# Kernel tuning notes

Hardware: AMD Instinct MI355X
Metric: run time of the kernel (lower is better)

Reference implementation:

```python
import jax, jax.numpy as jnp
import numpy as np

USR_NUM = 100000
D_IN = 32
D_HID = 32
D_MID = 16
D_OUT = 2
N_EDGES = 1600000
EPS = 1e-16  # matches torch_geometric.utils.softmax denominator eps


def _glorot(key, shape):
    fan_in, fan_out = shape[0], shape[1]
    lim = np.sqrt(6.0 / (fan_in + fan_out))
    return jax.random.uniform(key, shape, jnp.float32, -lim, lim)


def setup_inputs() -> dict:
    key = jax.random.key(0)
    ks = jax.random.split(key, 16)
    inp = {
        "edge_index": jax.random.randint(ks[0], (2, N_EDGES), 0, USR_NUM, dtype=jnp.int64)
        if jax.config.jax_enable_x64 else jax.random.randint(ks[0], (2, N_EDGES), 0, USR_NUM).astype(jnp.int32),
        "emb": jax.random.normal(ks[1], (USR_NUM, D_IN), jnp.float32),
        # conv1: TransformerConv(32 -> 32, heads=1)
        "Wq1": _glorot(ks[2], (D_IN, D_HID)), "bq1": jnp.zeros((D_HID,), jnp.float32),
        "Wk1": _glorot(ks[3], (D_IN, D_HID)), "bk1": jnp.zeros((D_HID,), jnp.float32),
        "Wv1": _glorot(ks[4], (D_IN, D_HID)), "bv1": jnp.zeros((D_HID,), jnp.float32),
        "Ws1": _glorot(ks[5], (D_IN, D_HID)), "bs1": jnp.zeros((D_HID,), jnp.float32),
        # conv2: TransformerConv(32 -> 16, heads=1)
        "Wq2": _glorot(ks[6], (D_HID, D_MID)), "bq2": jnp.zeros((D_MID,), jnp.float32),
        "Wk2": _glorot(ks[7], (D_HID, D_MID)), "bk2": jnp.zeros((D_MID,), jnp.float32),
        "Wv2": _glorot(ks[8], (D_HID, D_MID)), "bv2": jnp.zeros((D_MID,), jnp.float32),
        "Ws2": _glorot(ks[9], (D_HID, D_MID)), "bs2": jnp.zeros((D_MID,), jnp.float32),
        # output: Linear(16 -> 2)
        "Wo": _glorot(ks[10], (D_MID, D_OUT)), "bo": jnp.zeros((D_OUT,), jnp.float32),
    }
    return inp


def transformer_conv(x, src, dst, Wq, bq, Wk, bk, Wv, bv, Ws, bs, n_nodes):
    # edge (j=src -> i=dst): alpha_ij = softmax_i( <q_i, k_j> / sqrt(d) )
    d = Wq.shape[1]
    q = (x @ Wq + bq)[dst]          # [E, d]
    k = (x @ Wk + bk)[src]          # [E, d]
    v = (x @ Wv + bv)[src]          # [E, d]
    alpha = jnp.sum(q * k, axis=-1) / jnp.sqrt(jnp.float32(d))  # [E]
    # segment softmax over incoming edges of each destination node
    seg_max = jax.ops.segment_max(alpha, dst, num_segments=n_nodes)  # [N]
    e = jnp.exp(alpha - seg_max[dst])
    seg_sum = jax.ops.segment_sum(e, dst, num_segments=n_nodes)      # [N]
    w = e / (seg_sum[dst] + EPS)
    agg = jax.ops.segment_sum(v * w[:, None], dst, num_segments=n_nodes)  # [N, d]
    return agg + x @ Ws + bs  # root/skip connection (PyG default root_weight=True)


def reference(edge_index, emb,
              Wq1, bq1, Wk1, bk1, Wv1, bv1, Ws1, bs1,
              Wq2, bq2, Wk2, bk2, Wv2, bv2, Ws2, bs2,
              Wo, bo):
    src, dst = edge_index[0], edge_index[1]
    h = transformer_conv(emb, src, dst, Wq1, bq1, Wk1, bk1, Wv1, bv1, Ws1, bs1, USR_NUM)
    h = jax.nn.relu(h)
    h = transformer_conv(h, src, dst, Wq2, bq2, Wk2, bk2, Wv2, bv2, Ws2, bs2, USR_NUM)
    h = jax.nn.relu(h)
    return h @ Wo + bo  # [N, 2]
```

## Files before the change

### kernel.cpp

```cpp
#include <hip/hip_runtime.h>
#include <hip/hip_bf16.h>

typedef __hip_bfloat16 bf16;
typedef unsigned int uint;
typedef unsigned short ushort;

#define N_NODES 100000
#define N_EDGES_C 1600000
#define NSB 196
#define NSBP 200
#define SBCAP 10240
#define RND 2048
#define EPB (RND / 256)
#define NBIN 64
#define G_RAD ((N_EDGES_C + RND - 1) / RND)
#define NHB 392
#define HCAP 5632
#define NSLOT (NHB * 256)

__device__ __forceinline__ float ldf(const void* p, long i, int isbf) {
    return isbf ? __bfloat162float(((const bf16*)p)[i]) : ((const float*)p)[i];
}
__device__ __forceinline__ int ldidx(const int* ei, long pos, int is64) {
    return is64 ? ei[2 * pos] : ei[pos];
}
__device__ __forceinline__ ushort bfb(float x) {
    bf16 h = __float2bfloat16(x);
    return *(ushort*)&h;
}
__device__ __forceinline__ float bl(uint u) { return __uint_as_float(u << 16); }
__device__ __forceinline__ float bh(uint u) { return __uint_as_float(u & 0xFFFF0000u); }

__global__ void setup_kernel(
    const void* emb, const int* ei,
    const void* Wq1, const void* bq1, const void* Wk1, const void* bk1,
    const void* Wv1, const void* bv1, const void* Ws1, const void* bs1,
    const void* Wq2, const void* bq2, const void* Wk2, const void* bk2,
    const void* Wv2, const void* bv2, const void* Ws2, const void* bs2,
    const void* Wo, const void* bo,
    int* flags, float* wp1, float* bp1, float* wp2, float* bp2, float* woF,
    int* curSB) {
    __shared__ int sf0;
    int t = threadIdx.x;
    if (t < 64) {
        const bf16* pb = (const bf16*)emb;
        int bad = 0;
        for (int i = t; i < 256; i += 64) {
            float v = __bfloat162float(pb[i]);
            if (!(v > -1.0e6f && v < 1.0e6f)) bad++;
        }
        int nz = 0;
        for (int i = 2 * t + 1; i < 256; i += 128) nz += (ei[i] != 0) ? 1 : 0;
#pragma unroll
        for (int m = 32; m >= 1; m >>= 1) {
            bad += __shfl_xor(bad, m, 64);
            nz  += __shfl_xor(nz, m, 64);
        }
        if (t == 0) {
            int f0 = (bad <= 8) ? 1 : 0;
            flags[0] = f0;
            flags[1] = (nz == 0) ? 1 : 0;
            sf0 = f0;
        }
    }
    __syncthreads();
    int isbf = sf0;
    for (int i = t; i < 1024; i += 256) {
        wp1[i]        = ldf(Wq1, i, isbf);
        wp1[1024 + i] = ldf(Wk1, i, isbf);
        wp1[2048 + i] = ldf(Wv1, i, isbf);
        wp1[3072 + i] = ldf(Ws1, i, isbf);
    }
    for (int i = t; i < 512; i += 256) {
        wp2[i]        = ldf(Wq2, i, isbf);
        wp2[512 + i]  = ldf(Wk2, i, isbf);
        wp2[1024 + i] = ldf(Wv2, i, isbf);
        wp2[1536 + i] = ldf(Ws2, i, isbf);
    }
    if (t < 32) {
        bp1[t] = ldf(bq1, t, isbf); bp1[32 + t] = ldf(bk1, t, isbf);
        bp1[64 + t] = ldf(bv1, t, isbf); bp1[96 + t] = ldf(bs1, t, isbf);
        woF[t] = ldf(Wo, t, isbf);
    }
    if (t < 16) {
        bp2[t] = ldf(bq2, t, isbf); bp2[16 + t] = ldf(bk2, t, isbf);
        bp2[32 + t] = ldf(bv2, t, isbf); bp2[48 + t] = ldf(bs2, t, isbf);
    }
    if (t < 2) woF[32 + t] = ldf(bo, t, isbf);
    curSB[t] = 0;
}

template <int DOUT, bool RUNTIME_DTYPE>
__device__ __forceinline__ void node_linear_body(
    const void* __restrict__ X, const float* __restrict__ wpack,
    const float* __restrict__ bpack, const int* __restrict__ flags,
    float* __restrict__ q, ushort* __restrict__ kvb, float* __restrict__ s,
    int bid, float* __restrict__ sW, float* __restrict__ sbias, float* __restrict__ sX) {
    const int TPN = DOUT / 4;
    const int NPB = 256 / TPN;
    const int W_ELEMS = 4 * 32 * DOUT;

    const float4* wp4 = (const float4*)wpack;
    float4* sW4 = (float4*)sW;
    for (int i = threadIdx.x; i < W_ELEMS / 4; i += 256) sW4[i] = wp4[i];
    if (threadIdx.x < 4 * DOUT) sbias[threadIdx.x] = bpack[threadIdx.x];
    const int base = bid * NPB * 32;
    bool useBf = RUNTIME_DTYPE && (flags[0] != 0);
    if (useBf) {
        for (int i = threadIdx.x; i < NPB * 32; i += 256) {
            int g = base + i;
            float xv = (g < N_NODES * 32) ? __bfloat162float(((const bf16*)X)[g]) : 0.0f;
            sX[(i >> 5) * 36 + (i & 31)] = xv;
        }
    } else {
        for (int i = threadIdx.x; i < NPB * 32; i += 256) {
            int g = base + i;
            sX[(i >> 5) * 36 + (i & 31)] = (g < N_NODES * 32) ? ((const float*)X)[g] : 0.0f;
        }
    }
    __syncthreads();

    int l = threadIdx.x / TPN;
    int c4 = (threadIdx.x % TPN) * 4;
    int n = bid * NPB + l;
    if (n >= N_NODES) return;

    float xr[32];
#pragma unroll
    for (int j = 0; j < 8; j++) {
        float4 t4 = *(const float4*)&sX[l * 36 + 4 * j];
        xr[4 * j] = t4.x; xr[4 * j + 1] = t4.y; xr[4 * j + 2] = t4.z; xr[4 * j + 3] = t4.w;
    }
    float acc[4][4];
#pragma unroll
    for (int m = 0; m < 4; m++)
#pragma unroll
        for (int j = 0; j < 4; j++) acc[m][j] = sbias[m * DOUT + c4 + j];

#pragma unroll
    for (int t = 0; t < 32; t++) {
#pragma unroll
        for (int m = 0; m < 4; m++) {
            float4 w = *(const float4*)&sW[(m * 32 + t) * DOUT + c4];
            acc[m][0] += xr[t] * w.x;
            acc[m][1] += xr[t] * w.y;
            acc[m][2] += xr[t] * w.z;
            acc[m][3] += xr[t] * w.w;
        }
    }
    size_t o = (size_t)n * DOUT + c4;
    *(float4*)&q[o] = make_float4(acc[0][0], acc[0][1], acc[0][2], acc[0][3]);
    *(float4*)&s[o] = make_float4(acc[3][0], acc[3][1], acc[3][2], acc[3][3]);
    size_t okv = (size_t)n * 2 * DOUT + c4;
    ushort4 kp = make_ushort4(bfb(acc[1][0]), bfb(acc[1][1]), bfb(acc[1][2]), bfb(acc[1][3]));
    ushort4 vp = make_ushort4(bfb(acc[2][0]), bfb(acc[2][1]), bfb(acc[2][2]), bfb(acc[2][3]));
    *(ushort4*)&kvb[okv]        = kp;
    *(ushort4*)&kvb[okv + DOUT] = vp;
}

struct RadixS {
    int cnt[256]; int excl[256]; int gbase[NSBP];
    uint sVal[RND]; unsigned char sSb[RND];
};
struct LinS { float sW[4096]; float sbias[128]; float sX[32 * 36]; };
union alignas(16) FusedS { RadixS r; LinS l; };

__global__ void __launch_bounds__(256, 4) fused_ra_nl(
    const int* __restrict__ ei, const int* __restrict__ flags,
    int* __restrict__ curSB, uint* __restrict__ pairsSB,
    const void* __restrict__ X, const float* __restrict__ wpack,
    const float* __restrict__ bpack,
    float* __restrict__ q, ushort* __restrict__ kvb, float* __restrict__ s) {
    __shared__ FusedS u;
    if (blockIdx.x >= G_RAD) {
        node_linear_body<32, true>(X, wpack, bpack, flags, q, kvb, s,
                                   (int)blockIdx.x - G_RAD, u.l.sW, u.l.sbias, u.l.sX);
        return;
    }
    int* cnt = u.r.cnt; int* excl = u.r.excl; int* gbase = u.r.gbase;
    uint* sVal = u.r.sVal; unsigned char* sSb = u.r.sSb;
    const int is64 = flags[1];
    int t = threadIdx.x;
    cnt[t] = 0;
    __syncthreads();
    long base = (long)blockIdx.x * RND;

    int mySb[EPB]; int myRank[EPB]; uint myPk[EPB];
#pragma unroll
    for (int r = 0; r < EPB; r++) {
        long e = base + r * 256 + t;
        mySb[r] = -1;
        if (e < N_EDGES_C) {
            int d = ldidx(ei, (long)N_EDGES_C + e, is64);
            int src = ldidx(ei, e, is64);
            int sb = d >> 9;
            myPk[r] = (uint)src | ((uint)(d & 511) << 17);
            myRank[r] = atomicAdd(&cnt[sb], 1);
            mySb[r] = sb;
        }
    }
    __syncthreads();
    int v = cnt[t];
    excl[t] = v;
    __syncthreads();
    for (int off = 1; off < 256; off <<= 1) {
        int u2 = (t >= off) ? excl[t - off] : 0;
        __syncthreads();
        excl[t] += u2;
        __syncthreads();
    }
    int myExcl = excl[t] - v;
    __syncthreads();
    excl[t] = myExcl;
    __syncthreads();
#pragma unroll
    for (int r = 0; r < EPB; r++) {
        if (mySb[r] >= 0) {
            int pos = excl[mySb[r]] + myRank[r];
            sVal[pos] = myPk[r];
            sSb[pos] = (unsigned char)mySb[r];
        }
    }
    __syncthreads();
    if (t < NSBP)
        gbase[t] = (cnt[t] > 0) ? atomicAdd(&curSB[t], cnt[t]) : 0;
    __syncthreads();
    int tot = excl[NSBP - 1] + cnt[NSBP - 1];
    for (int i = t; i < tot; i += 256) {
        int sb = sSb[i];
        int gp = gbase[sb] + (i - excl[sb]);
        if (gp < SBCAP)
            pairsSB[(size_t)sb * SBCAP + gp] = sVal[i];
    }
}

__global__ void __launch_bounds__(256, 4) radix_b(
    const int* __restrict__ curSB, const uint* __restrict__ pairsSB,
    int* __restrict__ esrc,
    int* __restrict__ rowbeg, int* __restrict__ rowend,
    int* __restrict__ perm) {
    __shared__ uint sP[HCAP];
    __shared__ int dcnt[256], dexcl[256], dcur[256];
    __shared__ int hbin[NBIN], hbase[NBIN], hcur[NBIN];
    __shared__ int scnt;
    int sbh = blockIdx.x;
    int parent = sbh >> 1, half = sbh & 1;
    int t = threadIdx.x;
    int n = min(curSB[parent], SBCAP);
    dcnt[t] = 0; dcur[t] = 0;
    if (t < NBIN) { hbin[t] = 0; hcur[t] = 0; }
    if (t == 0) scnt = 0;
    perm[sbh * 256 + t] = -1;
    __syncthreads();
    const uint* srcp = pairsSB + (size_t)parent * SBCAP;
    for (int i = t; i < n; i += 256) {
        uint pk = srcp[i];
        if (((pk >> 25) & 1u) == (uint)half) {
            int m = atomicAdd(&scnt, 1);
            if (m < HCAP) sP[m] = pk;
            atomicAdd(&dcnt[(pk >> 17) & 255], 1);
        }
    }
    __syncthreads();
    int nc = min(scnt, HCAP);
    int v = dcnt[t];
    dexcl[t] = v;
    __syncthreads();
    for (int off = 1; off < 256; off <<= 1) {
        int u2 = (t >= off) ? dexcl[t - off] : 0;
        __syncthreads();
        dexcl[t] += u2;
        __syncthreads();
    }
    int myExcl = dexcl[t] - v;
    __syncthreads();
    dexcl[t] = myExcl;
    __syncthreads();
    const int EB = sbh * HCAP;
    int dst = sbh * 256 + t;
    int mybin = -1;
    if (dst < N_NODES) {
        int rb = min(myExcl, HCAP);
        int re = min(myExcl + v, HCAP);
        rowbeg[dst] = EB + rb;
        rowend[dst] = EB + re;
        mybin = min(v, NBIN - 1);
        atomicAdd(&hbin[mybin], 1);
    }
    __syncthreads();
    if (t < 64) {
        int hv = hbin[t];
        int sfx = hv;
#pragma unroll
        for (int off = 1; off < 64; off <<= 1) {
            int u2 = __shfl_down(sfx, off, 64);
            if (t + off < 64) sfx += u2;
        }
        hbase[t] = sfx - hv;
    }
    __syncthreads();
    if (dst < N_NODES) {
        int r = atomicAdd(&hcur[mybin], 1);
        perm[sbh * 256 + hbase[mybin] + r] = dst;
    }
    for (int i = t; i < nc; i += 256) {
        uint pk = sP[i];
        int j = (pk >> 17) & 255;
        int p2 = dexcl[j] + atomicAdd(&dcur[j], 1);
        if (p2 < HCAP) esrc[EB + p2] = (int)(pk & 0x1FFFF);
    }
}

template <int D, bool LAYER2>
__global__ void __launch_bounds__(256, 2) gather_attn(
                            const int* __restrict__ perm,
                            const int* __restrict__ rowbeg, const int* __restrict__ rowend,
                            const int* __restrict__ esrc,
                            const float* __restrict__ q, const ushort* __restrict__ kvb,
                            const float* __restrict__ s,
                            const float* __restrict__ wp2,
                            const float* __restrict__ bp2,
                            const float* __restrict__ woF,
                            const int* __restrict__ flags,
                            float* __restrict__ q2o, ushort* __restrict__ kvb2o,
                            float* __restrict__ s2o,
                            void* __restrict__ out) {
    const int LPD = D / 8;
    const int G = 64 / LPD;
    __shared__ float sW2[2048];
    __shared__ float sb2[64];
    __shared__ float sH[64 * 36];
    __shared__ int sDst[64];

    if constexpr (!LAYER2) {
        for (int i = threadIdx.x; i < 2048; i += 256) sW2[i] = wp2[i];
        if (threadIdx.x < 64) sb2[threadIdx.x] = bp2[threadIdx.x];
    }

    int lane = threadIdx.x & 63;
    int wave = (blockIdx.x * blockDim.x + threadIdx.x) >> 6;
    int g = lane / LPD;
    int c = lane % LPD;
    int idx = wave * G + g;
    if constexpr (LAYER2) {
        if (idx >= NSLOT) return;
    }
    int dst = perm[idx];
    if constexpr (LAYER2) {
        if (dst < 0) return;
    }
    bool alive = (dst >= 0);

    const float rsq = (D == 32) ? 0.17677669529663689f : 0.25f;
    float4 qa = make_float4(0.f, 0.f, 0.f, 0.f), qb = qa;
    int beg = 0, end = 0;
    if (alive) {
        qa = *(const float4*)(q + (size_t)dst * D + 8 * c);
        qb = *(const float4*)(q + (size_t)dst * D + 8 * c + 4);
        beg = rowbeg[dst]; end = rowend[dst];
    }

    const char* kvbase = (const char*)kvb;
    const int ROW = 4 * D;
    const int koff = 16 * c;
    const int voff = 2 * D + 16 * c;

    float sum0 = 0.f, sum1 = 0.f;
    float a0[8] = {0,0,0,0,0,0,0,0};
    float a1[8] = {0,0,0,0,0,0,0,0};

    uint4 kq[8], vq[8];
    int sn1[8];
#pragma unroll
    for (int r = 0; r < 8; r++) {
        int sn = (beg + r < end) ? esrc[beg + r] : 0;
        const char* p = kvbase + (size_t)sn * ROW;
        kq[r] = *(const uint4*)(p + koff);
        vq[r] = *(const uint4*)(p + voff);
    }
#pragma unroll
    for (int r = 0; r < 8; r++)
        sn1[r] = (beg + 8 + r < end) ? esrc[beg + 8 + r] : 0;

    for (int e = beg; e < end; e += 8) {
        uint4 kc[8], vc[8];
#pragma unroll
        for (int r = 0; r < 8; r++) { kc[r] = kq[r]; vc[r] = vq[r]; }
#pragma unroll
        for (int r = 0; r < 8; r++) {
            if (e + 8 + r < end) {
                const char* p = kvbase + (size_t)sn1[r] * ROW;
                kq[r] = *(const uint4*)(p + koff);
                vq[r] = *(const uint4*)(p + voff);
            }
        }
#pragma unroll
        for (int r = 0; r < 8; r++) {
            if (e + 16 + r < end) sn1[r] = esrc[e + 16 + r];
        }
#pragma unroll
        for (int r = 0; r < 8; r++) {
            if (e + r < end) {
                uint4 kA = kc[r], vA = vc[r];
                float pd = qa.x * bl(kA.x) + qa.y * bh(kA.x) + qa.z * bl(kA.y) + qa.w * bh(kA.y)
                         + qb.x * bl(kA.z) + qb.y * bh(kA.z) + qb.z * bl(kA.w) + qb.w * bh(kA.w);
#pragma unroll
                for (int m = LPD / 2; m >= 1; m >>= 1) pd += __shfl_xor(pd, m, LPD);
                float ex = __expf(fminf(fmaxf(pd * rsq, -80.0f), 80.0f));
                if (r & 1) {
                    sum1 += ex;
                    a1[0] += bl(vA.x) * ex; a1[1] += bh(vA.x) * ex;
                    a1[2] += bl(vA.y) * ex; a1[3] += bh(vA.y) * ex;
                    a1[4] += bl(vA.z) * ex; a1[5] += bh(vA.z) * ex;
                    a1[6] += bl(vA.w) * ex; a1[7] += bh(vA.w) * ex;
                } else {
                    sum0 += ex;
                    a0[0] += bl(vA.x) * ex; a0[1] += bh(vA.x) * ex;
                    a0[2] += bl(vA.y) * ex; a0[3] += bh(vA.y) * ex;
                    a0[4] += bl(vA.z) * ex; a0[5] += bh(vA.z) * ex;
                    a0[6] += bl(vA.w) * ex; a0[7] += bh(vA.w) * ex;
                }
            }
        }
    }
    float inv = 1.0f / (sum0 + sum1 + 1e-16f);
    float4 sa = make_float4(0.f, 0.f, 0.f, 0.f), sbv = sa;
    if (alive) {
        sa  = *(const float4*)(s + (size_t)dst * D + 8 * c);
        sbv = *(const float4*)(s + (size_t)dst * D + 8 * c + 4);
    }
    float h[8];
    h[0] = (a0[0] + a1[0]) * inv + sa.x;  h[1] = (a0[1] + a1[1]) * inv + sa.y;
    h[2] = (a0[2] + a1[2]) * inv + sa.z;  h[3] = (a0[3] + a1[3]) * inv + sa.w;
    h[4] = (a0[4] + a1[4]) * inv + sbv.x; h[5] = (a0[5] + a1[5]) * inv + sbv.y;
    h[6] = (a0[6] + a1[6]) * inv + sbv.z; h[7] = (a0[7] + a1[7]) * inv + sbv.w;
#pragma unroll
    for (int j = 0; j < 8; j++) h[j] = h[j] > 0.0f ? h[j] : 0.0f;

    if constexpr (!LAYER2) {
        int gl = (threadIdx.x >> 6) * G + g;
        if (alive) {
            *(float4*)&sH[gl * 36 + 8 * c]     = make_float4(h[0], h[1], h[2], h[3]);
            *(float4*)&sH[gl * 36 + 8 * c + 4] = make_float4(h[4], h[5], h[6], h[7]);
        }
        if (c == 0) sDst[gl] = dst;
        __syncthreads();
        int l = threadIdx.x >> 2;
        int c4 = (threadIdx.x & 3) * 4;
        int nd = sDst[l];
        if (nd >= 0) {
            float acc2[4][4];
#pragma unroll
            for (int m = 0; m < 4; m++)
#pragma unroll
                for (int j = 0; j < 4; j++) acc2[m][j] = sb2[m * 16 + c4 + j];
#pragma unroll
            for (int t2 = 0; t2 < 32; t2++) {
                float xv = sH[l * 36 + t2];
#pragma unroll
                for (int m = 0; m < 4; m++) {
                    float4 w = *(const float4*)&sW2[(m * 32 + t2) * 16 + c4];
                    acc2[m][0] += xv * w.x;
                    acc2[m][1] += xv * w.y;
                    acc2[m][2] += xv * w.z;
                    acc2[m][3] += xv * w.w;
                }
            }
            size_t o = (size_t)nd * 16 + c4;
            *(float4*)&q2o[o] = make_float4(acc2[0][0], acc2[0][1], acc2[0][2], acc2[0][3]);
            *(float4*)&s2o[o] = make_float4(acc2[3][0], acc2[3][1], acc2[3][2], acc2[3][3]);
            size_t okv = (size_t)nd * 32 + c4;
            ushort4 kp = make_ushort4(bfb(acc2[1][0]), bfb(acc2[1][1]), bfb(acc2[1][2]), bfb(acc2[1][3]));
            ushort4 vp = make_ushort4(bfb(acc2[2][0]), bfb(acc2[2][1]), bfb(acc2[2][2]), bfb(acc2[2][3]));
            *(ushort4*)&kvb2o[okv]      = kp;
            *(ushort4*)&kvb2o[okv + 16] = vp;
        }
    } else {
        float p0 = 0.f, p1 = 0.f;
#pragma unroll
        for (int j = 0; j < 8; j++) {
            p0 += h[j] * woF[(8 * c + j) * 2 + 0];
            p1 += h[j] * woF[(8 * c + j) * 2 + 1];
        }
#pragma unroll
        for (int m = LPD / 2; m >= 1; m >>= 1) {
            p0 += __shfl_xor(p0, m, LPD);
            p1 += __shfl_xor(p1, m, LPD);
        }
        if (c == 0) {
            float o0 = p0 + woF[32];
            float o1 = p1 + woF[33];
            if (flags[0]) {
                ((bf16*)out)[dst * 2 + 0] = __float2bfloat16(o0);
                ((bf16*)out)[dst * 2 + 1] = __float2bfloat16(o1);
            } else {
                ((float*)out)[dst * 2 + 0] = o0;
                ((float*)out)[dst * 2 + 1] = o1;
            }
        }
    }
}

extern "C" void kernel_launch(void* const* d_in, const int* in_sizes, int n_in,
                              void* d_out, int out_size, void* d_ws, size_t ws_size,
                              hipStream_t stream) {
    const int* ei  = (const int*)d_in[0];
    const void* emb = d_in[1];
    const void *Wq1 = d_in[2],  *bq1 = d_in[3];
    const void *Wk1 = d_in[4],  *bk1 = d_in[5];
    const void *Wv1 = d_in[6],  *bv1 = d_in[7];
    const void *Ws1 = d_in[8],  *bs1 = d_in[9];
    const void *Wq2 = d_in[10], *bq2 = d_in[11];
    const void *Wk2 = d_in[12], *bk2 = d_in[13];
    const void *Wv2 = d_in[14], *bv2 = d_in[15];
    const void *Ws2 = d_in[16], *bs2 = d_in[17];
    const void *Wo  = d_in[18], *bo  = d_in[19];

    const size_t ND   = (size_t)N_NODES * 32;
    const size_t ND16 = (size_t)N_NODES * 16;
    const size_t SBTOT = (size_t)NSB * SBCAP;
    const size_t ESRC_TOT = (size_t)NHB * HCAP;
    float* base   = (float*)d_ws;
    int*   flags  = (int*)base;
    float* wp1    = base + 64;
    float* bp1    = wp1 + 4096;
    float* wp2    = bp1 + 128;
    float* bp2    = wp2 + 2048;
    float* woF    = bp2 + 64;
    int*   curSB  = (int*)(woF + 64);
    int*   rowbeg = curSB + 256;
    int*   rowend = rowbeg + N_NODES;
    int*   perm   = rowend + N_NODES;
    float* p      = (float*)(perm + NSLOT);
    float* q      = p; p += ND;
    float* s      = p; p += ND;
    ushort* kvb   = (ushort*)p; p += ND;
    float* q2     = p; p += ND16;
    float* s2     = p; p += ND16;
    ushort* kvb2  = (ushort*)p; p += ND16;
    int*   esrc   = (int*)p; p += ESRC_TOT;
    uint*  pairsSB = (uint*)p;

    const int B = 256;
    const int gNL32  = (N_NODES + 31) / 32;
    const int gFused = G_RAD + gNL32;
    const int gG1    = NSLOT / 64;
    const int gG2    = NSLOT / 128;

    setup_kernel<<<1, B, 0, stream>>>(emb, ei,
        Wq1, bq1, Wk1, bk1, Wv1, bv1, Ws1, bs1,
        Wq2, bq2, Wk2, bk2, Wv2, bv2, Ws2, bs2, Wo, bo,
        flags, wp1, bp1, wp2, bp2, woF, curSB);

    fused_ra_nl<<<gFused, B, 0, stream>>>(ei, flags, curSB, pairsSB,
                                          emb, wp1, bp1, q, kvb, s);

    radix_b<<<NHB, B, 0, stream>>>(curSB, pairsSB, esrc, rowbeg, rowend, perm);

    gather_attn<32, false><<<gG1, B, 0, stream>>>(
        perm, rowbeg, rowend, esrc, q, kvb, s, wp2, bp2, nullptr, flags,
        q2, kvb2, s2, nullptr);

    gather_attn<16, true><<<gG2, B, 0, stream>>>(
        perm, rowbeg, rowend, esrc, q2, kvb2, s2, nullptr, nullptr, woF, flags,
        nullptr, nullptr, nullptr, d_out);
}
```

Measured before the change: 289.9 us.

## Sort edges within each destination by source chunk and shrink gather prefetch depth

The per-block radix pass now keys edges by destination and a 13-bit-shifted chunk of the source id, so each row's edges are ordered by source region. This should improve cache locality of the K/V gathers. The gather kernel's prefetch pipeline drops from 8-deep with separately prefetched indices to 4-deep, and its launch bounds hint is removed. In exchange, radix_b uses 16x larger shared histograms, drops to 2 blocks per CU, and does more per-thread scan work.

```diff
diff --git a/kernel.cpp b/kernel.cpp
--- a/kernel.cpp
+++ b/kernel.cpp
@@ -17,6 +17,8 @@
 #define NHB 392
 #define HCAP 5632
 #define NSLOT (NHB * 256)
+#define NCHUNK 16
+#define KEYN (256 * NCHUNK)
 
 __device__ __forceinline__ float ldf(const void* p, long i, int isbf) {
     return isbf ? __bfloat162float(((const bf16*)p)[i]) : ((const float*)p)[i];
@@ -234,20 +236,23 @@
     }
 }
 
-__global__ void __launch_bounds__(256, 4) radix_b(
+__global__ void __launch_bounds__(256, 2) radix_b(
     const int* __restrict__ curSB, const uint* __restrict__ pairsSB,
     int* __restrict__ esrc,
     int* __restrict__ rowbeg, int* __restrict__ rowend,
     int* __restrict__ perm) {
     __shared__ uint sP[HCAP];
-    __shared__ int dcnt[256], dexcl[256], dcur[256];
+    __shared__ int dcnt[KEYN];
+    __shared__ int dexcl[KEYN];
+    __shared__ int dcur[KEYN];
+    __shared__ int part[256];
     __shared__ int hbin[NBIN], hbase[NBIN], hcur[NBIN];
     __shared__ int scnt;
     int sbh = blockIdx.x;
     int parent = sbh >> 1, half = sbh & 1;
     int t = threadIdx.x;
     int n = min(curSB[parent], SBCAP);
-    dcnt[t] = 0; dcur[t] = 0;
+    for (int i = t; i < KEYN; i += 256) { dcnt[i] = 0; dcur[i] = 0; }
     if (t < NBIN) { hbin[t] = 0; hcur[t] = 0; }
     if (t == 0) scnt = 0;
     perm[sbh * 256 + t] = -1;
@@ -258,32 +263,36 @@
         if (((pk >> 25) & 1u) == (uint)half) {
             int m = atomicAdd(&scnt, 1);
             if (m < HCAP) sP[m] = pk;
-            atomicAdd(&dcnt[(pk >> 17) & 255], 1);
+            int key = (int)((pk >> 17) & 255) * NCHUNK + (int)((pk & 0x1FFFFu) >> 13);
+            atomicAdd(&dcnt[key], 1);
         }
     }
     __syncthreads();
     int nc = min(scnt, HCAP);
-    int v = dcnt[t];
-    dexcl[t] = v;
+    const int kb = t * NCHUNK;
+    int sum = 0;
+#pragma unroll
+    for (int j = 0; j < NCHUNK; j++) sum += dcnt[kb + j];
+    int v = sum;
+    part[t] = v;
     __syncthreads();
     for (int off = 1; off < 256; off <<= 1) {
-        int u2 = (t >= off) ? dexcl[t - off] : 0;
+        int u2 = (t >= off) ? part[t - off] : 0;
         __syncthreads();
-        dexcl[t] += u2;
+        part[t] += u2;
         __syncthreads();
     }
-    int myExcl = dexcl[t] - v;
-    __syncthreads();
-    dexcl[t] = myExcl;
+    int run = part[t] - v;
+    int myExcl = run;
+#pragma unroll
+    for (int j = 0; j < NCHUNK; j++) { dexcl[kb + j] = run; run += dcnt[kb + j]; }
     __syncthreads();
     const int EB = sbh * HCAP;
     int dst = sbh * 256 + t;
     int mybin = -1;
     if (dst < N_NODES) {
-        int rb = min(myExcl, HCAP);
-        int re = min(myExcl + v, HCAP);
-        rowbeg[dst] = EB + rb;
-        rowend[dst] = EB + re;
+        rowbeg[dst] = EB + min(myExcl, HCAP);
+        rowend[dst] = EB + min(myExcl + v, HCAP);
         mybin = min(v, NBIN - 1);
         atomicAdd(&hbin[mybin], 1);
     }
@@ -305,15 +314,14 @@
     }
     for (int i = t; i < nc; i += 256) {
         uint pk = sP[i];
-        int j = (pk >> 17) & 255;
-        int p2 = dexcl[j] + atomicAdd(&dcur[j], 1);
+        int key = (int)((pk >> 17) & 255) * NCHUNK + (int)((pk & 0x1FFFFu) >> 13);
+        int p2 = dexcl[key] + atomicAdd(&dcur[key], 1);
         if (p2 < HCAP) esrc[EB + p2] = (int)(pk & 0x1FFFF);
     }
 }
 
 template <int D, bool LAYER2>
-__global__ void __launch_bounds__(256, 2) gather_attn(
-                            const int* __restrict__ perm,
+__global__ void gather_attn(const int* __restrict__ perm,
                             const int* __restrict__ rowbeg, const int* __restrict__ rowend,
                             const int* __restrict__ esrc,
                             const float* __restrict__ q, const ushort* __restrict__ kvb,
@@ -369,37 +377,29 @@
     float a0[8] = {0,0,0,0,0,0,0,0};
     float a1[8] = {0,0,0,0,0,0,0,0};
 
-    uint4 kq[8], vq[8];
-    int sn1[8];
-#pragma unroll
-    for (int r = 0; r < 8; r++) {
+    uint4 kq[4], vq[4];
+#pragma unroll
+    for (int r = 0; r < 4; r++) {
         int sn = (beg + r < end) ? esrc[beg + r] : 0;
         const char* p = kvbase + (size_t)sn * ROW;
         kq[r] = *(const uint4*)(p + koff);
         vq[r] = *(const uint4*)(p + voff);
     }
-#pragma unroll
-    for (int r = 0; r < 8; r++)
-        sn1[r] = (beg + 8 + r < end) ? esrc[beg + 8 + r] : 0;
-
-    for (int e = beg; e < end; e += 8) {
-        uint4 kc[8], vc[8];
-#pragma unroll
-        for (int r = 0; r < 8; r++) { kc[r] = kq[r]; vc[r] = vq[r]; }
-#pragma unroll
-        for (int r = 0; r < 8; r++) {
-            if (e + 8 + r < end) {
-                const char* p = kvbase + (size_t)sn1[r] * ROW;
+
+    for (int e = beg; e < end; e += 4) {
+        uint4 kc[4], vc[4];
+#pragma unroll
+        for (int r = 0; r < 4; r++) { kc[r] = kq[r]; vc[r] = vq[r]; }
+#pragma unroll
+        for (int r = 0; r < 4; r++) {
+            if (e + 4 + r < end) {
+                const char* p = kvbase + (size_t)esrc[e + 4 + r] * ROW;
                 kq[r] = *(const uint4*)(p + koff);
                 vq[r] = *(const uint4*)(p + voff);
             }
         }
 #pragma unroll
-        for (int r = 0; r < 8; r++) {
-            if (e + 16 + r < end) sn1[r] = esrc[e + 16 + r];
-        }
-#pragma unroll
-        for (int r = 0; r < 8; r++) {
+        for (int r = 0; r < 4; r++) {
             if (e + r < end) {
                 uint4 kA = kc[r], vA = vc[r];
                 float pd = qa.x * bl(kA.x) + qa.y * bh(kA.x) + qa.z * bl(kA.y) + qa.w * bh(kA.y)
```

After: 265.0 us. 8.6% less time.
